# Performance work log

Hardware: AMD Instinct MI355X
Metric: run time of the kernel (lower is better)

Reference implementation:

```python
import jax, jax.numpy as jnp
import numpy as np

N, F, H, L = 1536, 32, 64, 3  # num_nodes, num_features, hidden, num_layers
NEG_SLOPE = 0.01
BN_EPS = 1e-5


def _lrelu(x):
    return jnp.where(x >= 0, x, NEG_SLOPE * x)


def _gin_layer(x, src, tgt, eps, w1, b1, w2, b2, g, be):
    # scatter-add aggregation: out[tgt] += x[src] (source_to_target flow)
    agg = jax.ops.segment_sum(x[src], tgt, num_segments=N)
    h = (1.0 + eps) * x + agg
    h = jax.nn.relu(h @ w1 + b1)
    h = jax.nn.relu(h @ w2 + b2)
    # BatchNorm1d, training-mode (batch statistics, biased variance)
    mean = jnp.mean(h, axis=0)
    var = jnp.mean((h - mean) ** 2, axis=0)
    return (h - mean) * jax.lax.rsqrt(var + BN_EPS) * g + be


def setup_inputs() -> dict:
    key = jax.random.key(0)
    ks = iter(jax.random.split(key, 40))

    def rn(shape, scale=0.05):
        return jax.random.normal(next(ks), shape, dtype=jnp.float32) * scale

    inp = {
        "x": rn((N, F), 1.0),
        "node_features": rn((N, F), 1.0),
        # conv1: F -> H
        "c1_eps": jnp.zeros((), jnp.float32),
        "c1_w1": rn((F, H)), "c1_b1": jnp.zeros((H,), jnp.float32),
        "c1_w2": rn((H, H)), "c1_b2": jnp.zeros((H,), jnp.float32),
        "c1_g": jnp.ones((H,), jnp.float32), "c1_be": jnp.zeros((H,), jnp.float32),
        # L-1 additional GIN convs: H -> H (stacked)
        "cv_eps": jnp.zeros((L - 1,), jnp.float32),
        "cv_w1": rn((L - 1, H, H)), "cv_b1": jnp.zeros((L - 1, H), jnp.float32),
        "cv_w2": rn((L - 1, H, H)), "cv_b2": jnp.zeros((L - 1, H), jnp.float32),
        "cv_g": jnp.ones((L - 1, H), jnp.float32), "cv_be": jnp.zeros((L - 1, H), jnp.float32),
        # projection head
        "lin1_w": rn((H, H)), "lin1_b": jnp.zeros((H,), jnp.float32),
        "lin2_w": rn((H, F)), "lin2_b": jnp.zeros((F,), jnp.float32),
        # edge predictor: 2F -> H -> H -> H -> 1
        "ep_w1": rn((2 * F, H)), "ep_b1": jnp.zeros((H,), jnp.float32),
        "ep_w2": rn((H, H)), "ep_b2": jnp.zeros((H,), jnp.float32),
        "ep_w3": rn((H, H)), "ep_b3": jnp.zeros((H,), jnp.float32),
        "ep_w4": rn((H, 1)), "ep_b4": jnp.zeros((1,), jnp.float32),
    }
    return inp


def reference(x, node_features, c1_eps, c1_w1, c1_b1, c1_w2, c1_b2, c1_g, c1_be,
              cv_eps, cv_w1, cv_b1, cv_w2, cv_b2, cv_g, cv_be,
              lin1_w, lin1_b, lin2_w, lin2_b,
              ep_w1, ep_b1, ep_w2, ep_b2, ep_w3, ep_b3, ep_w4, ep_b4):
    # complete-graph upper-triangular edge list (matches torch.combinations order)
    src, tgt = jnp.triu_indices(N, k=1)
    h = node_features  # forward ignores input x
    xinit = h
    h = _lrelu(_gin_layer(h, src, tgt, c1_eps, c1_w1, c1_b1, c1_w2, c1_b2, c1_g, c1_be))
    for i in range(L - 1):
        h = _lrelu(_gin_layer(h, src, tgt, cv_eps[i], cv_w1[i], cv_b1[i],
                              cv_w2[i], cv_b2[i], cv_g[i], cv_be[i]))
    h = _lrelu(h @ lin1_w + lin1_b)
    h = _lrelu(h @ lin2_w + lin2_b)
    h = h + xinit  # [N, F]

    # edge predictor: gather -> MLP -> sigmoid over E edges
    ef = jnp.concatenate([h[src], h[tgt]], axis=-1)  # [E, 2F]
    e = jax.nn.relu(ef @ ep_w1 + ep_b1)
    e = jax.nn.relu(e @ ep_w2 + ep_b2)
    e = jax.nn.relu(e @ ep_w3 + ep_b3)
    e = jax.nn.sigmoid(e @ ep_w4 + ep_b4)[:, 0]  # [E]

    probs = jnp.zeros((N, N), dtype=h.dtype)
    probs = probs.at[src, tgt].set(e).at[tgt, src].set(e)
    return probs
```

## Files before the change

### kernel.cpp

```cpp
#include <hip/hip_runtime.h>
#include <math.h>

#define NN 1536
#define FF 32
#define HH 64
#define EE (NN*(NN-1)/2)
#define EBLK 2493
#define BN_EPS 1e-5f
#define SLOPE 0.01f

typedef _Float16 v8h  __attribute__((ext_vector_type(8)));
typedef __fp16   v2hf __attribute__((ext_vector_type(2)));
typedef float    f32x4 __attribute__((ext_vector_type(4)));

union V8H { v8h v; v2hf h2[4]; float4 f4; };

__device__ __forceinline__ float lrelu_f(float v){ return v >= 0.f ? v : SLOPE*v; }


__global__ __launch_bounds__(256) void k_first(
    const float* __restrict__ nf, float* __restrict__ H,
    const float* __restrict__ pw2, const float* __restrict__ pw3,
    _Float16* __restrict__ pwf) {
  int bid = blockIdx.x, tid = threadIdx.x;
  if (bid >= 96) {
    int i = (bid - 96)*256 + tid;
    if (i < 8192) {
      int mat = i >> 12, r = i & 4095;
      int k = r >> 6, cout = r & 63;
      int m = cout >> 4, cc = cout & 15;
      int q, g, b;
      if (mat == 0) { q = k >> 5; g = (k >> 3) & 3; b = k & 7; }
      else { int mF = k >> 4; g = (k >> 2) & 3; int rr = k & 3; q = mF >> 1; b = ((mF & 1) << 2) | rr; }
      const float* W = mat ? pw3 : pw2;
      pwf[mat*4096 + ((q*4 + m)*64 + (g*16 + cc))*8 + b] = (_Float16)W[r];
    }
    return;
  }
  __shared__ float part[8][32];
  int c = tid & 31, y = tid >> 5;
  float s = nf[(bid*16 + y)*32 + c] + nf[(bid*16 + y + 8)*32 + c];
  part[y][c] = s;
  __syncthreads();
  if (y == 0) {
    float S = 0.f;
#pragma unroll
    for (int r = 0; r < 8; ++r) S += part[r][c];
    H[bid*64 + c] = S;
  }
}

__global__ __launch_bounds__(256) void k_bn(
    const float* __restrict__ z, const float* __restrict__ P,
    const float* __restrict__ gg, const float* __restrict__ be,
    float* __restrict__ hbuf, float* __restrict__ H) {
  __shared__ float sums[2][128];
  __shared__ float scl[64], sft[64];
  __shared__ float part[4][64];
  int tid = threadIdx.x, bid = blockIdx.x;
  {
    int c2 = tid & 127, half = tid >> 7;
    float S0 = 0.f, S1 = 0.f;
    int j0 = half*48;
    for (int j = j0; j < j0 + 48; j += 2) { S0 += P[j*128 + c2]; S1 += P[(j+1)*128 + c2]; }
    sums[half][c2] = S0 + S1;
  }
  __syncthreads();
  if (tid < 64) {
    float S = sums[0][tid] + sums[1][tid];
    float Q = sums[0][64 + tid] + sums[1][64 + tid];
    float m  = S * (1.f/NN);
    float iv = rsqrtf(Q * (1.f/NN) - m*m + BN_EPS);
    float sc = iv * gg[tid];
    scl[tid] = sc;
    sft[tid] = be[tid] - m*sc;
  }
  __syncthreads();
  int c = tid & 63, y = tid >> 6;
  float sc = scl[c], sh = sft[c];
  float hs = 0.f;
#pragma unroll
  for (int i = 0; i < 4; ++i) {
    int rr = y + 4*i;
    float h = lrelu_f(z[(bid*16 + rr)*64 + c]*sc + sh);
    hbuf[(bid*16 + rr)*64 + c] = h;
    hs += h;
  }
  part[y][c] = hs;
  __syncthreads();
  if (y == 0)
    H[bid*64 + c] = part[0][c] + part[1][c] + part[2][c] + part[3][c];
}

template<int DIN>
__global__ __launch_bounds__(512) void k_mmp(
    const float* __restrict__ hb, const float* __restrict__ H,
    const float* __restrict__ eps_p,
    const float* __restrict__ W1, const float* __restrict__ b1,
    const float* __restrict__ W2, const float* __restrict__ b2,
    float* __restrict__ zout, float* __restrict__ P) {
  __shared__ float W1s[DIN*64];
  __shared__ float W2s[4096];
  __shared__ float red[8][64];
  __shared__ float pf[64];
  __shared__ float hh[16][DIN];
  __shared__ float uls[16*DIN];
  __shared__ float t1s[16][64];
  __shared__ float pp[8][64], pq[8][64];
  int tid = threadIdx.x, bid = blockIdx.x;
  int c = tid & 63, y = tid >> 6;
  for (int i = tid; i < DIN*64; i += 512) W1s[i] = W1[i];
  for (int i = tid; i < 4096; i += 512)   W2s[i] = W2[i];

  {
    float s = 0.f;
    if (c < DIN) for (int j = y; j < bid; j += 8) s += H[j*64 + c];
    red[y][c] = s;
  }
  if (c < DIN) {
    hh[y][c]     = hb[(bid*16 + y)*DIN + c];
    hh[y + 8][c] = hb[(bid*16 + y + 8)*DIN + c];
  }
  __syncthreads();
  if (y == 0 && c < DIN) {
    float S = 0.f;
#pragma unroll
    for (int r = 0; r < 8; ++r) S += red[r][c];
    pf[c] = S;
  }
  __syncthreads();

  float e1 = 1.f + eps_p[0];
  if (c < DIN) {
    for (int rr = y; rr < 16; rr += 8) {
      float run = pf[c];
      for (int r2 = 0; r2 < rr; ++r2) run += hh[r2][c];
      uls[rr*DIN + c] = e1*hh[rr][c] + run;
    }
  }
  __syncthreads();

  float a0 = b1[c], a1 = a0;
  for (int k = 0; k < DIN; ++k) {
    float w = W1s[k*64 + c];
    a0 = fmaf(uls[y*DIN + k],       w, a0);
    a1 = fmaf(uls[(y + 8)*DIN + k], w, a1);
  }
  t1s[y][c]     = fmaxf(a0, 0.f);
  t1s[y + 8][c] = fmaxf(a1, 0.f);
  __syncthreads();

  float z0 = b2[c], z1 = z0;
  for (int k = 0; k < 64; ++k) {
    float w = W2s[k*64 + c];
    z0 = fmaf(t1s[y][k],     w, z0);
    z1 = fmaf(t1s[y + 8][k], w, z1);
  }
  z0 = fmaxf(z0, 0.f); z1 = fmaxf(z1, 0.f);
  zout[(bid*16 + y)*64 + c]     = z0;
  zout[(bid*16 + y + 8)*64 + c] = z1;

  pp[y][c] = z0 + z1;
  pq[y][c] = z0*z0 + z1*z1;
  __syncthreads();
  if (y == 0) {
    float S = 0.f, Q = 0.f;
#pragma unroll
    for (int r = 0; r < 8; ++r) { S += pp[r][c]; Q += pq[r][c]; }
    P[bid*128 + c]      = S;
    P[bid*128 + 64 + c] = Q;
  }
}

__global__ __launch_bounds__(512) void k_head2(
    const float* __restrict__ z, const float* __restrict__ P,
    const float* __restrict__ gg, const float* __restrict__ be,
    const float* __restrict__ l1w, const float* __restrict__ l1b,
    const float* __restrict__ l2w, const float* __restrict__ l2b,
    const float* __restrict__ nf,
    const float* __restrict__ epw1, const float* __restrict__ epb1,
    _Float16* __restrict__ Ah, _Float16* __restrict__ Bh) {
  __shared__ float W1s[4096];
  __shared__ float W2s[2048];
  __shared__ float Was[2048];
  __shared__ float Wbs[2048];
  __shared__ float sums[4][128];
  __shared__ float scratch[4096];
  __shared__ float scl[64], sft[64];
  int tid = threadIdx.x, c = tid & 63, y = tid >> 6;
  for (int i = tid; i < 4096; i += 512) W1s[i] = l1w[i];
  for (int i = tid; i < 2048; i += 512) { W2s[i] = l2w[i]; Was[i] = epw1[i]; Wbs[i] = epw1[2048 + i]; }

  {
    int c2 = tid & 127, q = tid >> 7;
    float S = 0.f;
    for (int j = q*24; j < q*24 + 24; ++j) S += P[j*128 + c2];
    sums[q][c2] = S;
  }
  __syncthreads();
  if (tid < 64) {
    float S = sums[0][tid] + sums[1][tid] + sums[2][tid] + sums[3][tid];
    float Q = sums[0][64+tid] + sums[1][64+tid] + sums[2][64+tid] + sums[3][64+tid];
    float m  = S * (1.f/NN);
    float iv = rsqrtf(Q * (1.f/NN) - m*m + BN_EPS);
    float sc = iv * gg[tid];
    scl[tid] = sc;
    sft[tid] = be[tid] - m*sc;
  }
  __syncthreads();

  float* t0 = scratch;
  float* t1 = scratch + 1024;
  float* t2 = scratch + 2048;
  int r0 = blockIdx.x*16;

  for (int rr = y; rr < 16; rr += 8)
    t0[rr*64 + c] = lrelu_f(z[(r0 + rr)*64 + c]*scl[c] + sft[c]);
  __syncthreads();
  {
    float a0 = l1b[c], a1 = a0;
    for (int k = 0; k < 64; ++k) {
      float w = W1s[k*64 + c];
      a0 = fmaf(t0[y*64 + k],       w, a0);
      a1 = fmaf(t0[(y + 8)*64 + k], w, a1);
    }
    t1[y*64 + c]       = lrelu_f(a0);
    t1[(y + 8)*64 + c] = lrelu_f(a1);
  }
  __syncthreads();
  if (c < 32) {
    float v0 = l2b[c], v1 = v0;
    for (int k = 0; k < 64; ++k) {
      float w = W2s[k*32 + c];
      v0 = fmaf(t1[y*64 + k],       w, v0);
      v1 = fmaf(t1[(y + 8)*64 + k], w, v1);
    }
    t2[y*32 + c]       = lrelu_f(v0) + nf[(r0 + y)*32 + c];
    t2[(y + 8)*32 + c] = lrelu_f(v1) + nf[(r0 + y + 8)*32 + c];
  }
  __syncthreads();
  {
    float av0 = epb1[c], av1 = av0;
    float bv0 = 0.f, bv1 = 0.f;
    for (int k = 0; k < 32; ++k) {
      float wa = Was[k*64 + c], wb = Wbs[k*64 + c];
      av0 = fmaf(t2[y*32 + k], wa, av0);       bv0 = fmaf(t2[y*32 + k], wb, bv0);
      av1 = fmaf(t2[(y + 8)*32 + k], wa, av1); bv1 = fmaf(t2[(y + 8)*32 + k], wb, bv1);
    }
    Ah[(r0 + y)*64 + c]     = (_Float16)av0;  Bh[(r0 + y)*64 + c]     = (_Float16)bv0;
    Ah[(r0 + y + 8)*64 + c] = (_Float16)av1;  Bh[(r0 + y + 8)*64 + c] = (_Float16)bv1;
  }
}

__global__ __launch_bounds__(256, 4) void k_edges_f16(
    const _Float16* __restrict__ Ah, const _Float16* __restrict__ Bh,
    const _Float16* __restrict__ Wf,
    const float* __restrict__ b2, const float* __restrict__ b3,
    const float* __restrict__ w4, const float* __restrict__ b4,
    float* __restrict__ out) {
  __shared__ _Float16 Wl[8192];
  int tid = threadIdx.x, wid = tid >> 6, lane = tid & 63;
  int c = lane & 15, g = lane >> 4;

  {
    const float4* src = (const float4*)Wf;
    float4* dst = (float4*)Wl;
    for (int i = tid; i < 1024; i += 256) dst[i] = src[i];
  }

  int w = blockIdx.x*4 + wid;
  int cum, kk, sbase;
  if (w < 1524) { cum = 0; kk = 12; sbase = 0; }
  else {
    cum = 1524; kk = 11; sbase = 127;
    while (kk > 1 && w >= cum + 128*kk) { cum += 128*kk; sbase += 128; --kk; }
  }
  int idx = w - cum;
  int q = idx / kk;
  int s = sbase + q;
  int t0 = s + 1 + ((idx - q*kk) << 7);

  f32x4 b2v[4], b3v[4];
  v2hf w4h[8];
  int g4 = g*4;
#pragma unroll
  for (int m = 0; m < 4; ++m) {
#pragma unroll
    for (int r = 0; r < 4; ++r) {
      int f = 16*m + g4 + r;
      b2v[m][r] = b2[f]; b3v[m][r] = b3[f];
    }
    v2hf wa = { (__fp16)w4[16*m + g4],     (__fp16)w4[16*m + g4 + 1] };
    v2hf wb = { (__fp16)w4[16*m + g4 + 2], (__fp16)w4[16*m + g4 + 3] };
    w4h[2*m] = wa; w4h[2*m + 1] = wb;
  }
  float b4v = b4[0];

  V8H zu; zu.f4 = make_float4(0.f, 0.f, 0.f, 0.f);
  const v8h vzero = zu.v;
  const v2hf z2 = { (__fp16)0.f, (__fp16)0.f };

  V8H a0, a1;
  a0.f4 = *(const float4*)(Ah + s*64 + g*8);
  a1.f4 = *(const float4*)(Ah + s*64 + 32 + g*8);

  int tl = t0 + c;
  V8H y0, y1;
  y0.f4 = *(const float4*)(Bh + tl*64 + g*8);
  y1.f4 = *(const float4*)(Bh + tl*64 + 32 + g*8);

  const v8h* wl = (const v8h*)Wl;
  __syncthreads();

  for (int it = 0; it < 8; ++it) {
    int tb = t0 + (it << 4);
    if (tb >= NN) break;
    int t = tb + c;

    V8H f0, f1;
    f0.v = __builtin_elementwise_max(a0.v + y0.v, vzero);
    f1.v = __builtin_elementwise_max(a1.v + y1.v, vzero);

    int tn = tb + 16 + c;
    y0.f4 = *(const float4*)(Bh + tn*64 + g*8);
    y1.f4 = *(const float4*)(Bh + tn*64 + 32 + g*8);

    __builtin_amdgcn_s_setprio(1);
    f32x4 acc[4];
#pragma unroll
    for (int m = 0; m < 4; ++m)
      acc[m] = __builtin_amdgcn_mfma_f32_16x16x32_f16(wl[m*64 + lane], f0.v, b2v[m], 0, 0, 0);
#pragma unroll
    for (int m = 0; m < 4; ++m)
      acc[m] = __builtin_amdgcn_mfma_f32_16x16x32_f16(wl[(4 + m)*64 + lane], f1.v, acc[m], 0, 0, 0);
    __builtin_amdgcn_s_setprio(0);

    V8H p0, p1;
#pragma unroll
    for (int m = 0; m < 2; ++m) {
      p0.h2[2*m]     = __builtin_elementwise_max(__builtin_amdgcn_cvt_pkrtz(acc[m][0],   acc[m][1]),   z2);
      p0.h2[2*m + 1] = __builtin_elementwise_max(__builtin_amdgcn_cvt_pkrtz(acc[m][2],   acc[m][3]),   z2);
      p1.h2[2*m]     = __builtin_elementwise_max(__builtin_amdgcn_cvt_pkrtz(acc[m+2][0], acc[m+2][1]), z2);
      p1.h2[2*m + 1] = __builtin_elementwise_max(__builtin_amdgcn_cvt_pkrtz(acc[m+2][2], acc[m+2][3]), z2);
    }

    __builtin_amdgcn_s_setprio(1);
    f32x4 acc3[4];
#pragma unroll
    for (int m = 0; m < 4; ++m)
      acc3[m] = __builtin_amdgcn_mfma_f32_16x16x32_f16(wl[512 + m*64 + lane], p0.v, b3v[m], 0, 0, 0);
#pragma unroll
    for (int m = 0; m < 4; ++m)
      acc3[m] = __builtin_amdgcn_mfma_f32_16x16x32_f16(wl[512 + (4 + m)*64 + lane], p1.v, acc3[m], 0, 0, 0);
    __builtin_amdgcn_s_setprio(0);

    float p = 0.f;
#pragma unroll
    for (int m = 0; m < 4; ++m) {
      v2hf l0 = __builtin_elementwise_max(
          __builtin_amdgcn_cvt_pkrtz(acc3[m][0], acc3[m][1]), z2);
      v2hf l1 = __builtin_elementwise_max(
          __builtin_amdgcn_cvt_pkrtz(acc3[m][2], acc3[m][3]), z2);
      p = __builtin_amdgcn_fdot2(l0, w4h[2*m],     p, false);
      p = __builtin_amdgcn_fdot2(l1, w4h[2*m + 1], p, false);
    }
    p += __shfl_xor(p, 16, 64);
    p += __shfl_xor(p, 32, 64);
    float ez = __builtin_amdgcn_exp2f(-1.44269504f * (p + b4v));
    float prob = __builtin_amdgcn_rcpf(1.f + ez);
    if (lane < 16 && t < NN) out[s*NN + t] = prob;
  }
}

__global__ __launch_bounds__(256) void k_mirror(float* __restrict__ out) {
  __shared__ float tile[32][33];
  int k = blockIdx.x;
  int bi = (int)((sqrtf(8.f*k + 1.f) - 1.f)*0.5f);
  while (bi*(bi + 1)/2 > k) --bi;
  while ((bi + 1)*(bi + 2)/2 <= k) ++bi;
  int bj = k - bi*(bi + 1)/2;
  int i0 = bi*32, j0 = bj*32;
  int tx = threadIdx.x & 31, ty = threadIdx.x >> 5;
#pragma unroll
  for (int r = 0; r < 4; ++r)
    tile[ty + r*8][tx] = out[(j0 + ty + r*8)*NN + i0 + tx];
  __syncthreads();
#pragma unroll
  for (int r = 0; r < 4; ++r) {
    int row = ty + r*8;
    int i = i0 + row, j = j0 + tx;
    if (bi > bj)      out[i*NN + j] = tile[tx][row];
    else if (i > j)   out[i*NN + j] = tile[tx][row];
    else if (i == j)  out[i*NN + j] = 0.f;
  }
}

extern "C" void kernel_launch(void* const* d_in, const int* in_sizes, int n_in,
                              void* d_out, int out_size, void* d_ws, size_t ws_size,
                              hipStream_t stream) {
  const float* nf     = (const float*)d_in[1];
  const float* c1_eps = (const float*)d_in[2];
  const float* c1_w1  = (const float*)d_in[3];
  const float* c1_b1  = (const float*)d_in[4];
  const float* c1_w2  = (const float*)d_in[5];
  const float* c1_b2  = (const float*)d_in[6];
  const float* c1_g   = (const float*)d_in[7];
  const float* c1_be  = (const float*)d_in[8];
  const float* cv_eps = (const float*)d_in[9];
  const float* cv_w1  = (const float*)d_in[10];
  const float* cv_b1  = (const float*)d_in[11];
  const float* cv_w2  = (const float*)d_in[12];
  const float* cv_b2  = (const float*)d_in[13];
  const float* cv_g   = (const float*)d_in[14];
  const float* cv_be  = (const float*)d_in[15];
  const float* lin1_w = (const float*)d_in[16];
  const float* lin1_b = (const float*)d_in[17];
  const float* lin2_w = (const float*)d_in[18];
  const float* lin2_b = (const float*)d_in[19];
  const float* ep_w1  = (const float*)d_in[20];
  const float* ep_b1  = (const float*)d_in[21];
  const float* ep_w2  = (const float*)d_in[22];
  const float* ep_b2  = (const float*)d_in[23];
  const float* ep_w3  = (const float*)d_in[24];
  const float* ep_b3  = (const float*)d_in[25];
  const float* ep_w4  = (const float*)d_in[26];
  const float* ep_b4  = (const float*)d_in[27];

  float* ws = (float*)d_ws;
  float* zA    = ws;
  float* zB    = zA + NN*64;
  float* hbuf  = zB + NN*64;
  float* H     = hbuf + NN*64;
  float* P     = H + 96*64;
  _Float16* Ah = (_Float16*)(P + 96*128);
  _Float16* Bh = Ah + NN*64;
  _Float16* Wf = Bh + NN*64;

  float* out = (float*)d_out;

  k_first<<<128, 256, 0, stream>>>(nf, H, ep_w2, ep_w3, Wf);
  k_mmp<32><<<96, 512, 0, stream>>>(nf, H, c1_eps, c1_w1, c1_b1, c1_w2, c1_b2, zA, P);

  k_bn<<<96, 256, 0, stream>>>(zA, P, c1_g, c1_be, hbuf, H);
  k_mmp<64><<<96, 512, 0, stream>>>(hbuf, H, cv_eps, cv_w1, cv_b1, cv_w2, cv_b2, zB, P);

  k_bn<<<96, 256, 0, stream>>>(zB, P, cv_g, cv_be, hbuf, H);
  k_mmp<64><<<96, 512, 0, stream>>>(hbuf, H, cv_eps + 1,
      cv_w1 + HH*HH, cv_b1 + HH, cv_w2 + HH*HH, cv_b2 + HH, zA, P);

  k_head2<<<96, 512, 0, stream>>>(zA, P, cv_g + HH, cv_be + HH,
                                  lin1_w, lin1_b, lin2_w, lin2_b, nf,
                                  ep_w1, ep_b1, Ah, Bh);

  k_edges_f16<<<EBLK, 256, 0, stream>>>(Ah, Bh, Wf, ep_b2, ep_b3, ep_w4, ep_b4, out);
  k_mirror<<<1176, 256, 0, stream>>>(out);
}
```

Before: 81.20 us.

## Switch edge MLP to 32x32x16 MFMA with register-resident weights

Replaces the 16x16x32 MFMA tiling in the edge kernel with 32x32x16 MFMAs, so each wave processes 32 target edges per iteration instead of 16. The weight matrices are held in registers, loaded directly from global memory, instead of being staged in LDS, and the host-side prepack layout is changed to match the new fragment order. This removes the LDS copy, the block barrier, one shuffle and the per-iteration LDS weight reads, and halves the loop trip count. In exchange the kernel uses more registers, so launch bounds drop from 4 to 2 blocks per SM and occupancy is lower.

```diff
diff --git a/kernel.cpp b/kernel.cpp
--- a/kernel.cpp
+++ b/kernel.cpp
@@ -9,14 +9,14 @@
 #define BN_EPS 1e-5f
 #define SLOPE 0.01f
 
-typedef _Float16 v8h  __attribute__((ext_vector_type(8)));
-typedef __fp16   v2hf __attribute__((ext_vector_type(2)));
+typedef _Float16 v8h   __attribute__((ext_vector_type(8)));
+typedef __fp16   v2hf  __attribute__((ext_vector_type(2)));
 typedef float    f32x4 __attribute__((ext_vector_type(4)));
+typedef float    f32x16 __attribute__((ext_vector_type(16)));
 
 union V8H { v8h v; v2hf h2[4]; float4 f4; };
 
 __device__ __forceinline__ float lrelu_f(float v){ return v >= 0.f ? v : SLOPE*v; }
-
 
 __global__ __launch_bounds__(256) void k_first(
     const float* __restrict__ nf, float* __restrict__ H,
@@ -28,12 +28,19 @@
     if (i < 8192) {
       int mat = i >> 12, r = i & 4095;
       int k = r >> 6, cout = r & 63;
-      int m = cout >> 4, cc = cout & 15;
-      int q, g, b;
-      if (mat == 0) { q = k >> 5; g = (k >> 3) & 3; b = k & 7; }
-      else { int mF = k >> 4; g = (k >> 2) & 3; int rr = k & 3; q = mF >> 1; b = ((mF & 1) << 2) | rr; }
+      int m = cout >> 5, c5 = cout & 31;
+      int frag, g2, b;
+      if (mat == 0) {
+        frag = k >> 4; g2 = (k >> 3) & 1; b = k & 7;
+      } else {
+        int kk = k & 31;
+        int q = kk >> 3, j = kk & 3;
+        g2 = (kk >> 2) & 1;
+        frag = (k >> 5)*2 + (q >> 1);
+        b = (q & 1)*4 + j;
+      }
       const float* W = mat ? pw3 : pw2;
-      pwf[mat*4096 + ((q*4 + m)*64 + (g*16 + cc))*8 + b] = (_Float16)W[r];
+      pwf[((mat*8 + m*4 + frag)*64 + (g2*32 + c5))*8 + b] = (_Float16)W[r];
     }
     return;
   }
@@ -252,21 +259,14 @@
   }
 }
 
-__global__ __launch_bounds__(256, 4) void k_edges_f16(
+__global__ __launch_bounds__(256, 2) void k_edges_f16(
     const _Float16* __restrict__ Ah, const _Float16* __restrict__ Bh,
     const _Float16* __restrict__ Wf,
     const float* __restrict__ b2, const float* __restrict__ b3,
     const float* __restrict__ w4, const float* __restrict__ b4,
     float* __restrict__ out) {
-  __shared__ _Float16 Wl[8192];
   int tid = threadIdx.x, wid = tid >> 6, lane = tid & 63;
-  int c = lane & 15, g = lane >> 4;
-
-  {
-    const float4* src = (const float4*)Wf;
-    float4* dst = (float4*)Wl;
-    for (int i = tid; i < 1024; i += 256) dst[i] = src[i];
-  }
+  int c5 = lane & 31, g2 = lane >> 5;
 
   int w = blockIdx.x*4 + wid;
   int cum, kk, sbase;
@@ -280,95 +280,110 @@
   int s = sbase + q;
   int t0 = s + 1 + ((idx - q*kk) << 7);
 
-  f32x4 b2v[4], b3v[4];
-  v2hf w4h[8];
-  int g4 = g*4;
-#pragma unroll
-  for (int m = 0; m < 4; ++m) {
-#pragma unroll
-    for (int r = 0; r < 4; ++r) {
-      int f = 16*m + g4 + r;
+  const v8h* wp = (const v8h*)Wf;
+  v8h wv2[8], wv3[8];
+#pragma unroll
+  for (int f = 0; f < 8; ++f) { wv2[f] = wp[f*64 + lane]; wv3[f] = wp[512 + f*64 + lane]; }
+
+  f32x16 b2v[2], b3v[2];
+#pragma unroll
+  for (int m = 0; m < 2; ++m)
+#pragma unroll
+    for (int r = 0; r < 16; ++r) {
+      int f = m*32 + (r & 3) + 8*(r >> 2) + 4*g2;
       b2v[m][r] = b2[f]; b3v[m][r] = b3[f];
     }
-    v2hf wa = { (__fp16)w4[16*m + g4],     (__fp16)w4[16*m + g4 + 1] };
-    v2hf wb = { (__fp16)w4[16*m + g4 + 2], (__fp16)w4[16*m + g4 + 3] };
-    w4h[2*m] = wa; w4h[2*m + 1] = wb;
-  }
+  v2hf w4h[16];
+#pragma unroll
+  for (int m = 0; m < 2; ++m)
+#pragma unroll
+    for (int i = 0; i < 8; ++i) {
+      int f = m*32 + 2*(i & 1) + 8*(i >> 1) + 4*g2;
+      v2hf wv = { (__fp16)w4[f], (__fp16)w4[f + 1] };
+      w4h[m*8 + i] = wv;
+    }
   float b4v = b4[0];
 
   V8H zu; zu.f4 = make_float4(0.f, 0.f, 0.f, 0.f);
   const v8h vzero = zu.v;
   const v2hf z2 = { (__fp16)0.f, (__fp16)0.f };
 
-  V8H a0, a1;
-  a0.f4 = *(const float4*)(Ah + s*64 + g*8);
-  a1.f4 = *(const float4*)(Ah + s*64 + 32 + g*8);
-
-  int tl = t0 + c;
-  V8H y0, y1;
-  y0.f4 = *(const float4*)(Bh + tl*64 + g*8);
-  y1.f4 = *(const float4*)(Bh + tl*64 + 32 + g*8);
-
-  const v8h* wl = (const v8h*)Wl;
-  __syncthreads();
-
-  for (int it = 0; it < 8; ++it) {
-    int tb = t0 + (it << 4);
+  V8H as[4];
+#pragma unroll
+  for (int f = 0; f < 4; ++f)
+    as[f].f4 = *(const float4*)(Ah + s*64 + f*16 + g2*8);
+
+  V8H yb[4];
+  {
+    int tl = t0 + c5;
+#pragma unroll
+    for (int f = 0; f < 4; ++f)
+      yb[f].f4 = *(const float4*)(Bh + tl*64 + f*16 + g2*8);
+  }
+
+  for (int it = 0; it < 4; ++it) {
+    int tb = t0 + (it << 5);
     if (tb >= NN) break;
-    int t = tb + c;
-
-    V8H f0, f1;
-    f0.v = __builtin_elementwise_max(a0.v + y0.v, vzero);
-    f1.v = __builtin_elementwise_max(a1.v + y1.v, vzero);
-
-    int tn = tb + 16 + c;
-    y0.f4 = *(const float4*)(Bh + tn*64 + g*8);
-    y1.f4 = *(const float4*)(Bh + tn*64 + 32 + g*8);
+    int t = tb + c5;
+
+    V8H x0, x1, x2, x3;
+    x0.v = __builtin_elementwise_max(as[0].v + yb[0].v, vzero);
+    x1.v = __builtin_elementwise_max(as[1].v + yb[1].v, vzero);
+    x2.v = __builtin_elementwise_max(as[2].v + yb[2].v, vzero);
+    x3.v = __builtin_elementwise_max(as[3].v + yb[3].v, vzero);
+
+    {
+      int tn = tb + 32 + c5;
+#pragma unroll
+      for (int f = 0; f < 4; ++f)
+        yb[f].f4 = *(const float4*)(Bh + tn*64 + f*16 + g2*8);
+    }
 
     __builtin_amdgcn_s_setprio(1);
-    f32x4 acc[4];
-#pragma unroll
-    for (int m = 0; m < 4; ++m)
-      acc[m] = __builtin_amdgcn_mfma_f32_16x16x32_f16(wl[m*64 + lane], f0.v, b2v[m], 0, 0, 0);
-#pragma unroll
-    for (int m = 0; m < 4; ++m)
-      acc[m] = __builtin_amdgcn_mfma_f32_16x16x32_f16(wl[(4 + m)*64 + lane], f1.v, acc[m], 0, 0, 0);
+    f32x16 acc0 = __builtin_amdgcn_mfma_f32_32x32x16_f16(wv2[0], x0.v, b2v[0], 0, 0, 0);
+    f32x16 acc1 = __builtin_amdgcn_mfma_f32_32x32x16_f16(wv2[4], x0.v, b2v[1], 0, 0, 0);
+    acc0 = __builtin_amdgcn_mfma_f32_32x32x16_f16(wv2[1], x1.v, acc0, 0, 0, 0);
+    acc1 = __builtin_amdgcn_mfma_f32_32x32x16_f16(wv2[5], x1.v, acc1, 0, 0, 0);
+    acc0 = __builtin_amdgcn_mfma_f32_32x32x16_f16(wv2[2], x2.v, acc0, 0, 0, 0);
+    acc1 = __builtin_amdgcn_mfma_f32_32x32x16_f16(wv2[6], x2.v, acc1, 0, 0, 0);
+    acc0 = __builtin_amdgcn_mfma_f32_32x32x16_f16(wv2[3], x3.v, acc0, 0, 0, 0);
+    acc1 = __builtin_amdgcn_mfma_f32_32x32x16_f16(wv2[7], x3.v, acc1, 0, 0, 0);
     __builtin_amdgcn_s_setprio(0);
 
-    V8H p0, p1;
-#pragma unroll
-    for (int m = 0; m < 2; ++m) {
-      p0.h2[2*m]     = __builtin_elementwise_max(__builtin_amdgcn_cvt_pkrtz(acc[m][0],   acc[m][1]),   z2);
-      p0.h2[2*m + 1] = __builtin_elementwise_max(__builtin_amdgcn_cvt_pkrtz(acc[m][2],   acc[m][3]),   z2);
-      p1.h2[2*m]     = __builtin_elementwise_max(__builtin_amdgcn_cvt_pkrtz(acc[m+2][0], acc[m+2][1]), z2);
-      p1.h2[2*m + 1] = __builtin_elementwise_max(__builtin_amdgcn_cvt_pkrtz(acc[m+2][2], acc[m+2][3]), z2);
+    V8H p0, p1, p2, p3;
+#pragma unroll
+    for (int i = 0; i < 4; ++i) {
+      p0.h2[i] = __builtin_elementwise_max(__builtin_amdgcn_cvt_pkrtz(acc0[2*i],     acc0[2*i + 1]),  z2);
+      p1.h2[i] = __builtin_elementwise_max(__builtin_amdgcn_cvt_pkrtz(acc0[8 + 2*i], acc0[9 + 2*i]),  z2);
+      p2.h2[i] = __builtin_elementwise_max(__builtin_amdgcn_cvt_pkrtz(acc1[2*i],     acc1[2*i + 1]),  z2);
+      p3.h2[i] = __builtin_elementwise_max(__builtin_amdgcn_cvt_pkrtz(acc1[8 + 2*i], acc1[9 + 2*i]),  z2);
     }
 
     __builtin_amdgcn_s_setprio(1);
-    f32x4 acc3[4];
-#pragma unroll
-    for (int m = 0; m < 4; ++m)
-      acc3[m] = __builtin_amdgcn_mfma_f32_16x16x32_f16(wl[512 + m*64 + lane], p0.v, b3v[m], 0, 0, 0);
-#pragma unroll
-    for (int m = 0; m < 4; ++m)
-      acc3[m] = __builtin_amdgcn_mfma_f32_16x16x32_f16(wl[512 + (4 + m)*64 + lane], p1.v, acc3[m], 0, 0, 0);
+    f32x16 ac0 = __builtin_amdgcn_mfma_f32_32x32x16_f16(wv3[0], p0.v, b3v[0], 0, 0, 0);
+    f32x16 ac1 = __builtin_amdgcn_mfma_f32_32x32x16_f16(wv3[4], p0.v, b3v[1], 0, 0, 0);
+    ac0 = __builtin_amdgcn_mfma_f32_32x32x16_f16(wv3[1], p1.v, ac0, 0, 0, 0);
+    ac1 = __builtin_amdgcn_mfma_f32_32x32x16_f16(wv3[5], p1.v, ac1, 0, 0, 0);
+    ac0 = __builtin_amdgcn_mfma_f32_32x32x16_f16(wv3[2], p2.v, ac0, 0, 0, 0);
+    ac1 = __builtin_amdgcn_mfma_f32_32x32x16_f16(wv3[6], p2.v, ac1, 0, 0, 0);
+    ac0 = __builtin_amdgcn_mfma_f32_32x32x16_f16(wv3[3], p3.v, ac0, 0, 0, 0);
+    ac1 = __builtin_amdgcn_mfma_f32_32x32x16_f16(wv3[7], p3.v, ac1, 0, 0, 0);
     __builtin_amdgcn_s_setprio(0);
 
     float p = 0.f;
 #pragma unroll
-    for (int m = 0; m < 4; ++m) {
+    for (int i = 0; i < 8; ++i) {
       v2hf l0 = __builtin_elementwise_max(
-          __builtin_amdgcn_cvt_pkrtz(acc3[m][0], acc3[m][1]), z2);
+          __builtin_amdgcn_cvt_pkrtz(ac0[2*i], ac0[2*i + 1]), z2);
       v2hf l1 = __builtin_elementwise_max(
-          __builtin_amdgcn_cvt_pkrtz(acc3[m][2], acc3[m][3]), z2);
-      p = __builtin_amdgcn_fdot2(l0, w4h[2*m],     p, false);
-      p = __builtin_amdgcn_fdot2(l1, w4h[2*m + 1], p, false);
-    }
-    p += __shfl_xor(p, 16, 64);
+          __builtin_amdgcn_cvt_pkrtz(ac1[2*i], ac1[2*i + 1]), z2);
+      p = __builtin_amdgcn_fdot2(l0, w4h[i],     p, false);
+      p = __builtin_amdgcn_fdot2(l1, w4h[8 + i], p, false);
+    }
     p += __shfl_xor(p, 32, 64);
     float ez = __builtin_amdgcn_exp2f(-1.44269504f * (p + b4v));
     float prob = __builtin_amdgcn_rcpf(1.f + ez);
-    if (lane < 16 && t < NN) out[s*NN + t] = prob;
+    if (g2 == 0 && t < NN) out[s*NN + t] = prob;
   }
 }
 
```

Result: slower. 86.47 us (+6.5%).
